# Performance work log

Measured on AMD Instinct MI355X. Metric: run time of the kernel, lower is better.

Reference implementation:

```python
import jax, jax.numpy as jnp
import numpy as np

B, CIN, COUT, K, H, W = 8, 256, 256, 3, 128, 128


def setup_inputs() -> dict:
    key = jax.random.key(0)
    k1, k2, k3 = jax.random.split(key, 3)
    return {
        "input_vector": jax.random.normal(k1, (B, CIN, H, W), dtype=jnp.float32),
        "style_vector": jax.random.normal(k2, (B, CIN), dtype=jnp.float32),
        "weight": jax.random.normal(k3, (COUT, CIN, K, K), dtype=jnp.float32),
    }


def reference(input_vector, style_vector, weight):
    b, cin, h, w = input_vector.shape
    cout, _, k, _ = weight.shape
    # per-sample modulated weights: (b, O, I, k, k)
    ws = weight[None, :, :, :, :] * style_vector[:, None, :, None, None]
    # NOTE: faithful to source - sum over dims [1,2,3] = (O, I, kh), NOT kw.
    demod = jax.lax.rsqrt(jnp.sum(ws * ws, axis=(1, 2, 3), keepdims=True) + 1e-8)  # (b,1,1,1,k)
    ws = (ws * demod).reshape(b * cout, cin, k, k)
    x = input_vector.reshape(1, b * cin, h, w)
    # get_same_padding(W, k, dilation=1, stride=1) = (k-1)//2
    pad = ((w - 1) * (1 - 1) + 1 * (k - 1)) // 2
    out = jax.lax.conv_general_dilated(
        x, ws,
        window_strides=(1, 1),
        padding=[(pad, pad), (pad, pad)],
        feature_group_count=b,
        dimension_numbers=("NCHW", "OIHW", "NCHW"),
    )
    out = out.reshape(b, cout, h, w)
    return jax.nn.leaky_relu(out, negative_slope=0.2)
```

## Files before the change

### kernel.cpp

```cpp
#include <hip/hip_runtime.h>
#include <hip/hip_bf16.h>

#define B_    8
#define CIN   256
#define COUT  256
#define H_    128
#define W_    128
#define HP    130
#define WP    130

#define OCT   128
#define TROWS 8
#define TCOLS 32
#define XROWS 10
#define XCOLS 34
#define XCH   1360
#define XCHP  1536
#define KHS   ((size_t)3 * COUT * CIN)

using bfrag = __attribute__((ext_vector_type(8))) short;
using f32x4 = __attribute__((ext_vector_type(4))) float;

#define ASM_VMCNT(n) asm volatile("s_waitcnt vmcnt(" #n ")" ::: "memory")
#define ASM_LGKM0()  asm volatile("s_waitcnt lgkmcnt(0)" ::: "memory")

__device__ __forceinline__ float leaky(float v) {
    return v >= 0.f ? v : 0.2f * v;
}

__device__ __forceinline__ unsigned short to_bf16(float v) {
    __hip_bfloat16 h = __float2bfloat16(v);
    return *(unsigned short*)&h;
}

__global__ void compute_S_kernel(const float* __restrict__ weight, float* __restrict__ S) {
    const int i = blockIdx.x;
    const int t = threadIdx.x;
    const float* wp = weight + ((size_t)t * CIN + i) * 9;
    float s0 = 0.f, s1 = 0.f, s2 = 0.f;
#pragma unroll
    for (int kh = 0; kh < 3; ++kh) {
        float a = wp[kh * 3 + 0], b = wp[kh * 3 + 1], c = wp[kh * 3 + 2];
        s0 = fmaf(a, a, s0); s1 = fmaf(b, b, s1); s2 = fmaf(c, c, s2);
    }
    __shared__ float red[3][256];
    red[0][t] = s0; red[1][t] = s1; red[2][t] = s2;
    __syncthreads();
    for (int off = 128; off > 0; off >>= 1) {
        if (t < off) {
            red[0][t] += red[0][t + off];
            red[1][t] += red[1][t + off];
            red[2][t] += red[2][t + off];
        }
        __syncthreads();
    }
    if (t == 0) {
        S[i * 3 + 0] = red[0][0];
        S[i * 3 + 1] = red[1][0];
        S[i * 3 + 2] = red[2][0];
    }
}

__global__ void compute_demod_kernel(const float* __restrict__ style,
                                     const float* __restrict__ S,
                                     float* __restrict__ demod) {
    const int b = blockIdx.x;
    const int t = threadIdx.x;
    float sv = style[b * CIN + t];
    float sv2 = sv * sv;
    float s0 = sv2 * S[t * 3 + 0];
    float s1 = sv2 * S[t * 3 + 1];
    float s2 = sv2 * S[t * 3 + 2];
    __shared__ float red[3][256];
    red[0][t] = s0; red[1][t] = s1; red[2][t] = s2;
    __syncthreads();
    for (int off = 128; off > 0; off >>= 1) {
        if (t < off) {
            red[0][t] += red[0][t + off];
            red[1][t] += red[1][t + off];
            red[2][t] += red[2][t + off];
        }
        __syncthreads();
    }
    if (t == 0) {
        demod[b * 3 + 0] = rsqrtf(red[0][0] + 1e-8f);
        demod[b * 3 + 1] = rsqrtf(red[1][0] + 1e-8f);
        demod[b * 3 + 2] = rsqrtf(red[2][0] + 1e-8f);
    }
}

__global__ void compute_wmodT_kernel(const float* __restrict__ weight,
                                     const float* __restrict__ style,
                                     const float* __restrict__ demod,
                                     unsigned short* __restrict__ wT) {
    const int bx = blockIdx.x;
    const int i  = threadIdx.x;
    const int o  = bx & (COUT - 1);
    const int j  = (bx >> 8) % 9;
    const int b  = bx / (9 * COUT);
    float w = weight[((size_t)o * CIN + i) * 9 + j];
    float m = style[b * CIN + i] * demod[b * 3 + (j % 3)];
    wT[(((size_t)(b * 9 + j) * COUT + o)) * CIN + i] = to_bf16(w * m);
}

__global__ __launch_bounds__(256) void transpose_kernel(const float* __restrict__ x,
                                                        unsigned short* __restrict__ xT) {
    const int bx = blockIdx.x;
    const int wtile = (bx & 3) * 32;
    const int itile = (bx >> 2) * 32;
    const int h = blockIdx.y;
    const int b = blockIdx.z;
    const int t = threadIdx.x;

    __shared__ float lt[32][33];

    {
        const int tw = t & 31, tr = t >> 5;
#pragma unroll
        for (int rr = 0; rr < 4; ++rr) {
            int il = tr + rr * 8;
            lt[il][tw] = x[(((size_t)b * CIN + itile + il) * H_ + h) * W_ + wtile + tw];
        }
    }
    __syncthreads();
    {
        const int il = t & 31, wr = t >> 5;
#pragma unroll
        for (int rr = 0; rr < 4; ++rr) {
            int wl = wr + rr * 8;
            xT[(((size_t)b * HP + (h + 1)) * WP + (wtile + wl + 1)) * CIN + itile + il] =
                to_bf16(lt[il][wl]);
        }
    }
}

__global__ void zero_border_kernel(unsigned short* __restrict__ xT) {
    const int b = blockIdx.x;
    const int r = blockIdx.y;
    const int t = threadIdx.x;
    int npix, base, stride;
    if (r == 0)      { npix = WP;  base = 0;                 stride = 1;  }
    else if (r == 1) { npix = WP;  base = (HP - 1) * WP;     stride = 1;  }
    else if (r == 2) { npix = 128; base = WP;                stride = WP; }
    else             { npix = 128; base = WP + (WP - 1);     stride = WP; }
    for (int idx = t; idx < npix * 32; idx += 256) {
        int p = idx >> 5, q = idx & 31;
        size_t off = ((size_t)b * HP * WP + base + (size_t)p * stride) * CIN;
        *(int4*)((unsigned short*)xT + off + q * 8) = (int4){0, 0, 0, 0};
    }
}

__global__ __launch_bounds__(256, 2) void conv_mfma_kernel(
    const unsigned short* __restrict__ xT,
    const unsigned short* __restrict__ wT,
    float* __restrict__ out)
{
    const int tid = threadIdx.x;
    const int lin = blockIdx.x;
    const int b    = lin & 7;
    const int rest = lin >> 3;
    const int oc0  = (rest & 1) * OCT;
    const int w0   = ((rest >> 1) & 3) * TCOLS;
    const int h0   = (rest >> 3) * TROWS;

    const int wid   = tid >> 6;
    const int lane  = tid & 63;
    const int wm    = wid >> 1;
    const int cw    = wid & 1;
    const int l15   = lane & 15;
    const int khalf = lane >> 4;

    __shared__ unsigned short lds_a[2][3 * OCT * 32];
    __shared__ unsigned short lds_x[XCHP * 8];

    const unsigned short* xb = xT + ((size_t)(b * HP + h0) * WP + w0) * CIN;
    const unsigned short* wb = wT + ((size_t)(b * 9) * COUT + oc0) * CIN;

    int offA[6];
#pragma unroll
    for (int j = 0; j < 6; ++j) {
        int c    = (wid * 6 + j) * 64 + lane;
        int slot = c & 3;
        int o    = (c >> 2) & 127;
        int kw   = c >> 9;
        offA[j] = (kw * COUT + o) * CIN + ((slot ^ ((o >> 1) & 3)) << 3);
    }
    int offX[6];
#pragma unroll
    for (int j = 0; j < 6; ++j) {
        int g  = (wid * 6 + j) * 64 + lane;
        int gg = g < XCH ? g : 0;
        int pix = gg >> 2, slot = gg & 3;
        int row = pix / XCOLS, col = pix - row * XCOLS;
        offX[j] = (row * WP + col) * CIN + ((slot ^ ((col >> 1) & 3)) << 3);
    }

    const int aoff = (wm * 64 + l15) * 32 + ((khalf ^ ((l15 >> 1) & 3)) << 3);
    int boff[3];
#pragma unroll
    for (int kw = 0; kw < 3; ++kw) {
        int col = cw * 16 + l15 + kw;
        boff[kw] = col * 32 + ((khalf ^ ((col >> 1) & 3)) << 3);
    }

    f32x4 acc[4][8];
#pragma unroll
    for (int m = 0; m < 4; ++m)
#pragma unroll
        for (int n = 0; n < 8; ++n) acc[m][n] = (f32x4){0.f, 0.f, 0.f, 0.f};

    auto stage_A = [&](unsigned short* dst, const unsigned short* wsrc) {
#pragma unroll
        for (int j = 0; j < 6; ++j) {
            __builtin_amdgcn_global_load_lds(
                (const __attribute__((address_space(1))) void*)(wsrc + offA[j]),
                (__attribute__((address_space(3))) void*)(dst + (wid * 6 + j) * 512),
                16, 0, 0);
        }
    };
    auto stage_X = [&](int i0) {
#pragma unroll
        for (int j = 0; j < 6; ++j) {
            __builtin_amdgcn_global_load_lds(
                (const __attribute__((address_space(1))) void*)(xb + offX[j] + i0),
                (__attribute__((address_space(3))) void*)(lds_x + (wid * 6 + j) * 512),
                16, 0, 0);
        }
    };

    auto compute = [&](int kh, const unsigned short* ab) {
        const unsigned short* ap = ab + aoff;
        const unsigned short* bp[3];
#pragma unroll
        for (int kw = 0; kw < 3; ++kw)
            bp[kw] = lds_x + (size_t)kh * XCOLS * 32 + boff[kw];

        bfrag aF[2][4];
        bfrag bs[3];
#pragma unroll
        for (int m = 0; m < 4; ++m)
            aF[0][m] = *(const bfrag*)(ap + (size_t)m * 16 * 32);
        bs[0] = *(const bfrag*)(bp[0]);
        bs[1] = *(const bfrag*)(bp[0] + (size_t)XCOLS * 32);
        __builtin_amdgcn_sched_group_barrier(0x100, 6, 0);

        __builtin_amdgcn_s_setprio(1);
#pragma unroll
        for (int g = 0; g < 24; ++g) {
            const int kw = g >> 3, n = g & 7;
            int nr = 0;
            if (g <= 21) {
                const int k2 = g + 2, n2 = k2 & 7, kw2 = k2 >> 3;
                bs[k2 % 3] = *(const bfrag*)(bp[kw2] + (size_t)n2 * XCOLS * 32);
                ++nr;
            }
            if (n >= 1 && n <= 4 && kw < 2) {
                const int mj = n - 1;
                aF[(kw + 1) & 1][mj] =
                    *(const bfrag*)(ap + ((size_t)(kw + 1) * 128 + mj * 16) * 32);
                ++nr;
            }
            if (nr == 1) __builtin_amdgcn_sched_group_barrier(0x100, 1, 0);
            if (nr == 2) __builtin_amdgcn_sched_group_barrier(0x100, 2, 0);
#pragma unroll
            for (int m = 0; m < 4; ++m)
                acc[m][n] = __builtin_amdgcn_mfma_f32_16x16x32_bf16(
                    aF[kw & 1][m], bs[g % 3], acc[m][n], 0, 0, 0);
            __builtin_amdgcn_sched_group_barrier(0x8, 4, 0);
        }
        __builtin_amdgcn_s_setprio(0);
    };

    stage_X(0);
    stage_A(lds_a[0], wb);

#define PHASE(KH, CUR, NXT, PRE_OFF)                                  \
    stage_A((NXT), wb + (PRE_OFF));                                   \
    ASM_VMCNT(6);                                                     \
    __builtin_amdgcn_s_barrier();                                     \
    __builtin_amdgcn_sched_barrier(0);                                \
    compute((KH), (CUR));                                             \
    ASM_LGKM0();                                                      \
    __builtin_amdgcn_s_barrier();                                     \
    __builtin_amdgcn_sched_barrier(0);

#pragma unroll 1
    for (int c = 0; c < 8; ++c) {
        unsigned short* pa = lds_a[c & 1];
        unsigned short* pb = lds_a[(c & 1) ^ 1];
        const size_t i0  = (size_t)c * 32;
        const size_t i0n = (size_t)((c + 1) & 7) * 32;

        PHASE(0, pa, pb, KHS + i0)
        PHASE(1, pb, pa, 2 * KHS + i0)
        PHASE(2, pa, pb, i0n)
        if (c < 7) stage_X((int)i0n);
    }
#undef PHASE
    ASM_VMCNT(0);

#pragma unroll
    for (int m = 0; m < 4; ++m) {
#pragma unroll
        for (int n = 0; n < 8; ++n) {
            int h = h0 + n;
            int w = w0 + cw * 16 + l15;
#pragma unroll
            for (int r = 0; r < 4; ++r) {
                int oc = oc0 + wm * 64 + m * 16 + khalf * 4 + r;
                out[(((size_t)b * COUT + oc) * H_ + h) * W_ + w] = leaky(acc[m][n][r]);
            }
        }
    }
}

extern "C" void kernel_launch(void* const* d_in, const int* in_sizes, int n_in,
                              void* d_out, int out_size, void* d_ws, size_t ws_size,
                              hipStream_t stream) {
    const float* x      = (const float*)d_in[0];
    const float* style  = (const float*)d_in[1];
    const float* weight = (const float*)d_in[2];
    float* out = (float*)d_out;

    float* S     = (float*)d_ws;
    float* demod = (float*)((char*)d_ws + 4096);
    unsigned short* wT = (unsigned short*)((char*)d_ws + 8192);
    unsigned short* xT = (unsigned short*)((char*)d_ws + 9445376);

    compute_S_kernel<<<CIN, 256, 0, stream>>>(weight, S);
    compute_demod_kernel<<<B_, 256, 0, stream>>>(style, S, demod);
    compute_wmodT_kernel<<<B_ * 9 * COUT, 256, 0, stream>>>(weight, style, demod, wT);
    transpose_kernel<<<dim3(32, H_, B_), 256, 0, stream>>>(x, xT);
    zero_border_kernel<<<dim3(B_, 4), 256, 0, stream>>>(xT);

    conv_mfma_kernel<<<dim3(1024), 256, 0, stream>>>(xT, wT, out);
}
```

Measured before the change: 184.7 us.

## Reorder conv phases by kernel column to reuse each B fragment across three kernel rows

Each pipeline phase now covers one kernel column kw with all three kernel rows, instead of one kernel row with all three columns. Each loaded input-row B fragment feeds the MFMAs of up to three output rows, which cuts LDS reads of the input tile. All three kh A fragments are held in registers, which raises register pressure. The hand-placed sched_group_barrier interleaving is gone, X offsets are recomputed per stage, and a full vmcnt(0) wait is added before the first phase.

```diff
diff --git a/kernel.cpp b/kernel.cpp
--- a/kernel.cpp
+++ b/kernel.cpp
@@ -16,7 +16,7 @@
 #define XCOLS 34
 #define XCH   1360
 #define XCHP  1536
-#define KHS   ((size_t)3 * COUT * CIN)
+#define CCS   ((size_t)COUT * CIN)
 
 using bfrag = __attribute__((ext_vector_type(8))) short;
 using f32x4 = __attribute__((ext_vector_type(4))) float;
@@ -182,25 +182,9 @@
         int c    = (wid * 6 + j) * 64 + lane;
         int slot = c & 3;
         int o    = (c >> 2) & 127;
-        int kw   = c >> 9;
-        offA[j] = (kw * COUT + o) * CIN + ((slot ^ ((o >> 1) & 3)) << 3);
-    }
-    int offX[6];
-#pragma unroll
-    for (int j = 0; j < 6; ++j) {
-        int g  = (wid * 6 + j) * 64 + lane;
-        int gg = g < XCH ? g : 0;
-        int pix = gg >> 2, slot = gg & 3;
-        int row = pix / XCOLS, col = pix - row * XCOLS;
-        offX[j] = (row * WP + col) * CIN + ((slot ^ ((col >> 1) & 3)) << 3);
-    }
-
-    const int aoff = (wm * 64 + l15) * 32 + ((khalf ^ ((l15 >> 1) & 3)) << 3);
-    int boff[3];
-#pragma unroll
-    for (int kw = 0; kw < 3; ++kw) {
-        int col = cw * 16 + l15 + kw;
-        boff[kw] = col * 32 + ((khalf ^ ((col >> 1) & 3)) << 3);
+        int kh   = c >> 9;
+        offA[j] = (int)((size_t)(kh * 3) * CCS) + o * CIN
+                  + ((slot ^ ((o >> 1) & 3)) << 3);
     }
 
     f32x4 acc[4][8];
@@ -221,65 +205,67 @@
     auto stage_X = [&](int i0) {
 #pragma unroll
         for (int j = 0; j < 6; ++j) {
+            int g  = (wid * 6 + j) * 64 + lane;
+            int gg = g < XCH ? g : 0;
+            int pix = gg >> 2, slot = gg & 3;
+            int row = pix / XCOLS, col = pix - row * XCOLS;
+            int ofx = (row * WP + col) * CIN + ((slot ^ ((col >> 1) & 3)) << 3);
             __builtin_amdgcn_global_load_lds(
-                (const __attribute__((address_space(1))) void*)(xb + offX[j] + i0),
+                (const __attribute__((address_space(1))) void*)(xb + ofx + i0),
                 (__attribute__((address_space(3))) void*)(lds_x + (wid * 6 + j) * 512),
                 16, 0, 0);
         }
     };
 
-    auto compute = [&](int kh, const unsigned short* ab) {
-        const unsigned short* ap = ab + aoff;
-        const unsigned short* bp[3];
-#pragma unroll
-        for (int kw = 0; kw < 3; ++kw)
-            bp[kw] = lds_x + (size_t)kh * XCOLS * 32 + boff[kw];
-
-        bfrag aF[2][4];
+    const int aoff = (wm * 64 + l15) * 32 + ((khalf ^ ((l15 >> 1) & 3)) << 3);
+
+    auto compute = [&](int kw, const unsigned short* ab) {
+        const int col = cw * 16 + l15 + kw;
+        const unsigned short* bp = lds_x + col * 32 + ((khalf ^ ((col >> 1) & 3)) << 3);
+
+        bfrag aF[3][4];
+#pragma unroll
+        for (int kh = 0; kh < 3; ++kh)
+#pragma unroll
+            for (int m = 0; m < 4; ++m)
+                aF[kh][m] = *(const bfrag*)(ab + aoff + ((size_t)kh * 128 + m * 16) * 32);
+
         bfrag bs[3];
-#pragma unroll
-        for (int m = 0; m < 4; ++m)
-            aF[0][m] = *(const bfrag*)(ap + (size_t)m * 16 * 32);
-        bs[0] = *(const bfrag*)(bp[0]);
-        bs[1] = *(const bfrag*)(bp[0] + (size_t)XCOLS * 32);
-        __builtin_amdgcn_sched_group_barrier(0x100, 6, 0);
+        bs[0] = *(const bfrag*)(bp);
+        bs[1] = *(const bfrag*)(bp + (size_t)XCOLS * 32);
 
         __builtin_amdgcn_s_setprio(1);
 #pragma unroll
-        for (int g = 0; g < 24; ++g) {
-            const int kw = g >> 3, n = g & 7;
-            int nr = 0;
-            if (g <= 21) {
-                const int k2 = g + 2, n2 = k2 & 7, kw2 = k2 >> 3;
-                bs[k2 % 3] = *(const bfrag*)(bp[kw2] + (size_t)n2 * XCOLS * 32);
-                ++nr;
+        for (int r = 0; r < 10; ++r) {
+            if (r < 8)
+                bs[(r + 2) % 3] = *(const bfrag*)(bp + (size_t)(r + 2) * XCOLS * 32);
+            const bfrag bv = bs[r % 3];
+#pragma unroll
+            for (int kh = 0; kh < 3; ++kh) {
+                const int n = r - kh;
+                if (n >= 0 && n < 8) {
+#pragma unroll
+                    for (int m = 0; m < 4; ++m)
+                        acc[m][n] = __builtin_amdgcn_mfma_f32_16x16x32_bf16(
+                            aF[kh][m], bv, acc[m][n], 0, 0, 0);
+                }
             }
-            if (n >= 1 && n <= 4 && kw < 2) {
-                const int mj = n - 1;
-                aF[(kw + 1) & 1][mj] =
-                    *(const bfrag*)(ap + ((size_t)(kw + 1) * 128 + mj * 16) * 32);
-                ++nr;
-            }
-            if (nr == 1) __builtin_amdgcn_sched_group_barrier(0x100, 1, 0);
-            if (nr == 2) __builtin_amdgcn_sched_group_barrier(0x100, 2, 0);
-#pragma unroll
-            for (int m = 0; m < 4; ++m)
-                acc[m][n] = __builtin_amdgcn_mfma_f32_16x16x32_bf16(
-                    aF[kw & 1][m], bs[g % 3], acc[m][n], 0, 0, 0);
-            __builtin_amdgcn_sched_group_barrier(0x8, 4, 0);
         }
         __builtin_amdgcn_s_setprio(0);
     };
 
     stage_X(0);
     stage_A(lds_a[0], wb);
-
-#define PHASE(KH, CUR, NXT, PRE_OFF)                                  \
+    ASM_VMCNT(0);
+    __builtin_amdgcn_s_barrier();
+    __builtin_amdgcn_sched_barrier(0);
+
+#define PHASE(KW, CUR, NXT, PRE_OFF)                                  \
     stage_A((NXT), wb + (PRE_OFF));                                   \
     ASM_VMCNT(6);                                                     \
     __builtin_amdgcn_s_barrier();                                     \
     __builtin_amdgcn_sched_barrier(0);                                \
-    compute((KH), (CUR));                                             \
+    compute((KW), (CUR));                                             \
     ASM_LGKM0();                                                      \
     __builtin_amdgcn_s_barrier();                                     \
     __builtin_amdgcn_sched_barrier(0);
@@ -291,8 +277,8 @@
         const size_t i0  = (size_t)c * 32;
         const size_t i0n = (size_t)((c + 1) & 7) * 32;
 
-        PHASE(0, pa, pb, KHS + i0)
-        PHASE(1, pb, pa, 2 * KHS + i0)
+        PHASE(0, pa, pb, 1 * CCS + i0)
+        PHASE(1, pb, pa, 2 * CCS + i0)
         PHASE(2, pa, pb, i0n)
         if (c < 7) stage_X((int)i0n);
     }
```

New measurement: 182.2 us. No clear change (-1.4%).
